# Kernel tuning notes

Measured on AMD Instinct MI355X. Metric: run time of the kernel, lower is better.

Reference implementation:

```python
import jax, jax.numpy as jnp
import numpy as np

N_NODES = 100000


def gcn_conv(x, W, b, row, col, n_nodes):
    # Symmetric GCN normalization without self-loops (add_self_loops=False):
    # deg[i] = number of incoming edges at target i (edge_weight = 1)
    deg = jax.ops.segment_sum(jnp.ones(row.shape[0], dtype=x.dtype), col,
                              num_segments=n_nodes)
    dinv = jnp.where(deg > 0, jax.lax.rsqrt(jnp.maximum(deg, 1.0)), 0.0)
    norm = dinv[row] * dinv[col]  # [E]
    h = x @ W                      # [N, out] linear transform first (PyG order)
    msg = h[row] * norm[:, None]   # gather + scale, [E, out]
    out = jax.ops.segment_sum(msg, col, num_segments=n_nodes)  # scatter-add
    return out + b


def setup_inputs() -> dict:
    key = jax.random.key(0)
    k1, k2, k3, k4, k5, k6 = jax.random.split(key, 6)
    n, in_c, hid, out_c, e = N_NODES, 128, 32, 16, 3200000
    x = jax.random.normal(k1, (n, in_c), dtype=jnp.float32)
    edge_index = jax.random.randint(k2, (2, e), 0, n, dtype=jnp.int64)
    # Glorot-style init for GCN weights, zeros bias (PyG default)
    W1 = jax.random.normal(k3, (in_c, hid), dtype=jnp.float32) / np.sqrt(in_c)
    b1 = jnp.zeros((hid,), dtype=jnp.float32)
    W2 = jax.random.normal(k4, (hid, out_c), dtype=jnp.float32) / np.sqrt(hid)
    b2 = jnp.zeros((out_c,), dtype=jnp.float32)
    return {"x": x, "edge_index": edge_index, "W1": W1, "b1": b1,
            "W2": W2, "b2": b2}


def reference(x, edge_index, W1, b1, W2, b2):
    row, col = edge_index[0], edge_index[1]
    h = gcn_conv(x, W1, b1, row, col, N_NODES)
    h = jax.nn.relu(h)
    out = gcn_conv(h, W2, b2, row, col, N_NODES)
    return (out, 0)
```

## Files before the change

### kernel.cpp

```cpp
#include <hip/hip_runtime.h>


#define WAVE 64
#define BN2 512
#define NBMAX 256
#define CHUNK 8192

typedef _Float16 f16;

__global__ void bucket_count_kernel(const int* __restrict__ col, int* __restrict__ gcnt,
                                    int E, int nb) {
    __shared__ int h[NBMAX];
    for (int i = threadIdx.x; i < nb; i += blockDim.x) h[i] = 0;
    __syncthreads();
    for (int e = blockIdx.x * blockDim.x + threadIdx.x; e < E; e += gridDim.x * blockDim.x)
        atomicAdd(&h[col[e] >> 9], 1);
    __syncthreads();
    for (int i = threadIdx.x; i < nb; i += blockDim.x)
        if (h[i]) atomicAdd(&gcnt[i], h[i]);
}

__global__ void bucket_scan_kernel(const int* __restrict__ cnt, int* __restrict__ bptr,
                                   int* __restrict__ gcur, int nb, int* __restrict__ gpcur,
                                   f16* __restrict__ hlo, f16* __restrict__ hhi,
                                   f16* __restrict__ h2t, int nzr) {
    int lane = threadIdx.x;
    if (lane == 0) gpcur[0] = 0;
    if (lane < 16)      hlo[(size_t)nzr * 16 + lane]        = (f16)0.f;
    else if (lane < 32) hhi[(size_t)nzr * 16 + (lane - 16)] = (f16)0.f;
    else if (lane < 48) h2t[(size_t)nzr * 16 + (lane - 32)] = (f16)0.f;
    int carry = 0;
    for (int base = 0; base < nb; base += WAVE) {
        int i = base + lane;
        int orig = (i < nb) ? cnt[i] : 0;
        int v = orig;
#pragma unroll
        for (int off = 1; off < WAVE; off <<= 1) {
            int t = __shfl_up(v, off, WAVE);
            if (lane >= off) v += t;
        }
        if (i < nb) { bptr[i] = carry + v - orig; gcur[i] = carry + v - orig; }
        carry += __shfl(v, WAVE - 1, WAVE);
    }
    if (lane == 0) bptr[nb] = carry;
}

__global__ void __launch_bounds__(512)
partition_kernel(const int* __restrict__ row, const int* __restrict__ col,
                 int* __restrict__ gcursor, unsigned* __restrict__ packed,
                 int E, int nb) {
    __shared__ int hist[NBMAX], excl[NBMAX], cursor[NBMAX], baseoff[NBMAX];
    __shared__ unsigned stage[CHUNK];
    int chunk0 = blockIdx.x * CHUNK;
    int cn = E - chunk0; if (cn > CHUNK) cn = CHUNK;
    for (int i = threadIdx.x; i < nb; i += blockDim.x) hist[i] = 0;
    __syncthreads();
    for (int i = threadIdx.x; i < cn; i += blockDim.x)
        atomicAdd(&hist[col[chunk0 + i] >> 9], 1);
    __syncthreads();
    if (threadIdx.x < WAVE) {
        int lane = threadIdx.x, carry = 0;
        for (int base = 0; base < nb; base += WAVE) {
            int i = base + lane;
            int orig = (i < nb) ? hist[i] : 0;
            int v = orig;
#pragma unroll
            for (int off = 1; off < WAVE; off <<= 1) {
                int t = __shfl_up(v, off, WAVE);
                if (lane >= off) v += t;
            }
            if (i < nb) { excl[i] = carry + v - orig; cursor[i] = carry + v - orig; }
            carry += __shfl(v, WAVE - 1, WAVE);
        }
    }
    __syncthreads();
    for (int b = threadIdx.x; b < nb; b += blockDim.x) {
        int c = hist[b];
        baseoff[b] = c ? atomicAdd(&gcursor[b], c) : 0;
    }
    __syncthreads();
    for (int i = threadIdx.x; i < cn; i += blockDim.x) {
        int c = col[chunk0 + i], r = row[chunk0 + i];
        int b = c >> 9;
        int pos = atomicAdd(&cursor[b], 1);
        stage[pos] = ((unsigned)r << 9) | (unsigned)(c & (BN2 - 1));
    }
    __syncthreads();
    int wave = threadIdx.x >> 6, lane = threadIdx.x & 63, nw = blockDim.x >> 6;
    for (int b = wave; b < nb; b += nw) {
        int c = hist[b]; if (!c) continue;
        int s = excl[b], d = baseoff[b];
        for (int k = lane; k < c; k += WAVE) packed[d + k] = stage[s + k];
    }
}

__global__ void __launch_bounds__(512)
sort_kernel(const int* __restrict__ bptr, const unsigned* __restrict__ packed,
            int* __restrict__ srcs, int2* __restrict__ pse,
            float* __restrict__ dinv, int* __restrict__ gpcur,
            int n, int nb, int E) {
    __shared__ int hist[BN2], pex[BN2], cur[BN2];
    __shared__ int pbase_s;
    int b = blockIdx.x;
    int start = bptr[b], end = bptr[b + 1];
    for (int i = threadIdx.x; i < BN2; i += blockDim.x) { hist[i] = 0; cur[i] = 0; }
    __syncthreads();
    for (int k = start + threadIdx.x; k < end; k += blockDim.x)
        atomicAdd(&hist[packed[k] & (BN2 - 1)], 1);
    __syncthreads();
    if (threadIdx.x < WAVE) {
        int lane = threadIdx.x, carry = 0;
#pragma unroll
        for (int base = 0; base < BN2; base += WAVE) {
            int i = base + lane;
            int pd = (hist[i] + 15) & ~15;
            int v = pd;
#pragma unroll
            for (int off = 1; off < WAVE; off <<= 1) {
                int t = __shfl_up(v, off, WAVE);
                if (lane >= off) v += t;
            }
            pex[i] = carry + v - pd;
            carry += __shfl(v, WAVE - 1, WAVE);
        }
        if (lane == 0) pbase_s = atomicAdd(gpcur, carry);
    }
    __syncthreads();
    int pbase = pbase_s;
    for (int i = threadIdx.x; i < BN2; i += blockDim.x) {
        int node = b * BN2 + i;
        if (node < n) {
            int d = hist[i], pd = (d + 15) & ~15;
            int ps = pbase + pex[i];
            pse[node]  = d ? make_int2(ps, ps + pd) : make_int2(0, 0);
            dinv[node] = d ? rsqrtf((float)d) : 0.f;
            for (int k = d; k < pd; ++k) srcs[ps + k] = n;
        }
    }
    __syncthreads();
    for (int k = start + threadIdx.x; k < end; k += blockDim.x) {
        unsigned p = packed[k];
        int lc = p & (BN2 - 1);
        int pos = atomicAdd(&cur[lc], 1);
        srcs[pbase + pex[lc] + pos] = (int)(p >> 9);
    }
}

template <int INC, int OUTC, int JT, bool SPLIT>
__global__ void __launch_bounds__(256, 4)
dense_kernel(const float* __restrict__ x, const float* __restrict__ W,
             const float* __restrict__ dinv, f16* __restrict__ hlo,
             f16* __restrict__ hhi, int n) {
    const int LSTR = INC + 4;
    const int SP   = 256 / JT;
    const int NT   = SP * 2;
    __shared__ float Wt[OUTC * LSTR];
    for (int i = threadIdx.x; i < INC * OUTC; i += 256) {
        int k = i / OUTC, j = i % OUTC;
        Wt[j * LSTR + k] = W[i];
    }
    __syncthreads();
    const int jg = threadIdx.x % JT;
    const int sp = threadIdx.x / JT;
    int base = blockIdx.x * NT;
    int n0 = base + sp;
    int n1 = base + sp + SP;
    int n0c = n0 < n ? n0 : n - 1;
    int n1c = n1 < n ? n1 : n - 1;
    const float4* xr0 = (const float4*)(x + (size_t)n0c * INC);
    const float4* xr1 = (const float4*)(x + (size_t)n1c * INC);
    float a[2][4] = {{0.f, 0.f, 0.f, 0.f}, {0.f, 0.f, 0.f, 0.f}};
#pragma unroll 4
    for (int k4 = 0; k4 < INC / 4; ++k4) {
        float4 v0 = xr0[k4];
        float4 v1 = xr1[k4];
#pragma unroll
        for (int u = 0; u < 4; ++u) {
            float4 w = *(const float4*)(Wt + (jg + u * JT) * LSTR + 4 * k4);
            a[0][u] = fmaf(v0.x, w.x, fmaf(v0.y, w.y, fmaf(v0.z, w.z, fmaf(v0.w, w.w, a[0][u]))));
            a[1][u] = fmaf(v1.x, w.x, fmaf(v1.y, w.y, fmaf(v1.z, w.z, fmaf(v1.w, w.w, a[1][u]))));
        }
    }
#pragma unroll
    for (int pair = 0; pair < 2; ++pair) {
        int nn = pair ? n1 : n0;
        if (nn < n) {
            float d = dinv[nn];
#pragma unroll
            for (int u = 0; u < 4; ++u) {
                int c = jg + u * JT;
                f16* t;
                if (SPLIT) t = (c < 16) ? (hlo + (size_t)nn * 16 + c)
                               : (hhi + (size_t)nn * 16 + (c - 16));
                else       t = hlo + (size_t)nn * OUTC + c;
                *t = (f16)(a[pair][u] * d);
            }
        }
    }
}

#define GLD(s) (*(const f16*)(hb + (((unsigned)(s) << 5) + j2)))

template <bool RELU>
__global__ void __launch_bounds__(256)
csr_agg16x2_kernel(const int2* __restrict__ pse, const int* __restrict__ srcs,
                   const float* __restrict__ dinv, const f16* __restrict__ tlo,
                   const f16* __restrict__ thi, const float* __restrict__ bias,
                   float* __restrict__ out, int ostride, int hg, int n, int tailidx) {
    int bid = blockIdx.x;
    int pass = (bid >= hg) ? 1 : 0;
    const f16* hs = pass ? thi : tlo;
    int ocol = pass << 4;
    int bip = bid - pass * hg;
    int lane = threadIdx.x & 63;
    int wid  = threadIdx.x >> 6;
    int j  = lane & 15;
    int eo = lane >> 4;
    if (tailidx >= 0 && bid == 0 && threadIdx.x == 0) out[tailidx] = 0.f;
    int n0 = (bip * 4 + wid) * 2;
    if (n0 >= n) return;
    int n1 = n0 + 1;
    bool v1 = n1 < n;
    int4 se = *(const int4*)(pse + n0);
    int nb0 = (se.y - se.x) >> 4;
    int nb1 = v1 ? ((se.w - se.z) >> 4) : 0;
    float dv0 = dinv[n0];
    float dv1 = v1 ? dinv[n1] : 0.f;
    float bj = bias[ocol + j];
    size_t ob0 = (size_t)n0 * ostride + ocol + j;
    size_t ob1 = (size_t)n1 * ostride + ocol + j;
    int MAXB = nb0 > nb1 ? nb0 : nb1;
    if (MAXB == 0) {
        float v = bj;
        if (RELU) v = v > 0.f ? v : 0.f;
        if (eo == 0) out[ob0] = v;
        else if (eo == 1 && v1) out[ob1] = v;
        return;
    }
    const unsigned j2 = (unsigned)(j << 1);
    const char* hb = (const char*)hs;
    const int4* P0 = (const int4*)(srcs + se.x) + eo;
    const int4* P1 = (const int4*)(srcs + (v1 ? se.z : se.x)) + eo;
    int nc0 = nb0 > 1 ? nb0 : 1;
    int nc1 = nb1 > 1 ? nb1 : 1;
    int4 sA0 = P0[0];
    int4 sA1 = P1[0];
    f16 h0 = GLD(sA0.x), h1 = GLD(sA0.y), h2 = GLD(sA0.z), h3 = GLD(sA0.w);
    f16 h4 = GLD(sA1.x), h5 = GLD(sA1.y), h6 = GLD(sA1.z), h7 = GLD(sA1.w);
    int4 sB0 = P0[(nc0 > 1 ? 1 : 0) * 4];
    int4 sB1 = P1[(nc1 > 1 ? 1 : 0) * 4];
    float acc0 = 0.f, acc1 = 0.f, acc2 = 0.f, acc3 = 0.f;
    for (int b = 0; b < MAXB - 1; ++b) {
        f16 g0 = GLD(sB0.x), g1 = GLD(sB0.y), g2 = GLD(sB0.z), g3 = GLD(sB0.w);
        f16 g4 = GLD(sB1.x), g5 = GLD(sB1.y), g6 = GLD(sB1.z), g7 = GLD(sB1.w);
        int x0 = (b + 2) < nc0 ? (b + 2) : nc0 - 1;
        int x1 = (b + 2) < nc1 ? (b + 2) : nc1 - 1;
        int4 t0 = P0[x0 * 4];
        int4 t1 = P1[x1 * 4];
        float m0 = b < nb0 ? 1.f : 0.f;
        float m1 = b < nb1 ? 1.f : 0.f;
        acc0 = fmaf(m0, (float)h0, acc0);
        acc1 = fmaf(m0, (float)h1, acc1);
        acc0 = fmaf(m0, (float)h2, acc0);
        acc1 = fmaf(m0, (float)h3, acc1);
        acc2 = fmaf(m1, (float)h4, acc2);
        acc3 = fmaf(m1, (float)h5, acc3);
        acc2 = fmaf(m1, (float)h6, acc2);
        acc3 = fmaf(m1, (float)h7, acc3);
        h0 = g0; h1 = g1; h2 = g2; h3 = g3;
        h4 = g4; h5 = g5; h6 = g6; h7 = g7;
        sB0 = t0; sB1 = t1;
    }
    {
        float m0 = (MAXB - 1) < nb0 ? 1.f : 0.f;
        float m1 = (MAXB - 1) < nb1 ? 1.f : 0.f;
        acc0 = fmaf(m0, (float)h0, acc0);
        acc1 = fmaf(m0, (float)h1, acc1);
        acc0 = fmaf(m0, (float)h2, acc0);
        acc1 = fmaf(m0, (float)h3, acc1);
        acc2 = fmaf(m1, (float)h4, acc2);
        acc3 = fmaf(m1, (float)h5, acc3);
        acc2 = fmaf(m1, (float)h6, acc2);
        acc3 = fmaf(m1, (float)h7, acc3);
    }
    float accA = acc0 + acc1;
    float accB = acc2 + acc3;
    accA += __shfl_xor(accA, 16, WAVE);
    accA += __shfl_xor(accA, 32, WAVE);
    accB += __shfl_xor(accB, 16, WAVE);
    accB += __shfl_xor(accB, 32, WAVE);
    if (eo == 0) {
        float v = accA * dv0 + bj;
        if (RELU) v = v > 0.f ? v : 0.f;
        out[ob0] = v;
    } else if (eo == 1 && v1) {
        float v = accB * dv1 + bj;
        if (RELU) v = v > 0.f ? v : 0.f;
        out[ob1] = v;
    }
}

extern "C" void kernel_launch(void* const* d_in, const int* in_sizes, int n_in,
                              void* d_out, int out_size, void* d_ws, size_t ws_size,
                              hipStream_t stream) {
    const float* x  = (const float*)d_in[0];
    const int*   ei = (const int*)d_in[1];
    const float* W1 = (const float*)d_in[2];
    const float* b1 = (const float*)d_in[3];
    const float* W2 = (const float*)d_in[4];
    const float* b2 = (const float*)d_in[5];

    const int IN_C = 128, HID = 32, OC = 16;
    const int N = in_sizes[0] / IN_C;
    const int E = in_sizes[1] / 2;
    const int* row = ei;
    const int* col = ei + E;
    const int NB = (N + BN2 - 1) / BN2;

    char* base = (char*)d_ws;
    size_t off = 0;
    auto carve = [&](size_t bytes) -> char* {
        char* p = base + off;
        off = (off + bytes + 255) & ~(size_t)255;
        return p;
    };
    int*      gcnt  = (int*)     carve((size_t)NB * 4);
    int*      bptr  = (int*)     carve((size_t)(NB + 1) * 4);
    int*      gcur  = (int*)     carve((size_t)NB * 4);
    int*      gpcur = (int*)     carve(8);
    float*    dinv  = (float*)   carve((size_t)N * 4);
    int2*     pse   = (int2*)    carve((size_t)(N + 2) * 8);
    unsigned* packed= (unsigned*)carve((size_t)E * 4);
    int*      srcsP = (int*)     carve(((size_t)E + (size_t)N * 32 + 256) * 4);
    f16*      hlo   = (f16*)     carve((size_t)(N + 1) * 16 * 2);
    f16*      hhi   = (f16*)     carve((size_t)(N + 1) * 16 * 2);
    f16*      h2t   = (f16*)     carve((size_t)(N + 1) * 16 * 2);
    float*    bufB  = (float*)   carve((size_t)N * HID * 4);
    (void)ws_size; (void)n_in;

    float* outp = (float*)d_out;

    hipMemsetAsync(gcnt, 0, (size_t)NB * 4, stream);
    bucket_count_kernel<<<512, 256, 0, stream>>>(col, gcnt, E, NB);
    bucket_scan_kernel<<<1, 64, 0, stream>>>(gcnt, bptr, gcur, NB, gpcur, hlo, hhi, h2t, N);
    partition_kernel<<<(E + CHUNK - 1) / CHUNK, 512, 0, stream>>>(row, col, gcur, packed, E, NB);
    sort_kernel<<<NB, 512, 0, stream>>>(bptr, packed, srcsP, pse, dinv, gpcur, N, NB, E);

    int npb = 8;
    int g2  = (N + npb - 1) / npb;

    {
        const int NT = (256 / 8) * 2;
        dense_kernel<128, 32, 8, true><<<(N + NT - 1) / NT, 256, 0, stream>>>(x, W1, dinv, hlo, hhi, N);
        csr_agg16x2_kernel<true><<<2 * g2, 256, 0, stream>>>(
            pse, srcsP, dinv, hlo, hhi, b1, bufB, HID, g2, N, -1);
    }
    {
        const int NT = (256 / 4) * 2;
        dense_kernel<32, 16, 4, false><<<(N + NT - 1) / NT, 256, 0, stream>>>(bufB, W2, dinv, h2t, nullptr, N);
        int tailidx = (out_size > N * OC) ? (N * OC) : -1;
        csr_agg16x2_kernel<false><<<g2, 256, 0, stream>>>(
            pse, srcsP, dinv, h2t, h2t, b2, outp, OC, g2, N, tailidx);
    }
}
```

Measured before the change: 192.0 us.

## Merge split layer-1 feature halves into one 32-column fp16 aggregation pass

After: 182.3 us. 5.0% less time.

```diff
diff --git a/kernel.cpp b/kernel.cpp
--- a/kernel.cpp
+++ b/kernel.cpp
@@ -22,12 +22,10 @@
 
 __global__ void bucket_scan_kernel(const int* __restrict__ cnt, int* __restrict__ bptr,
                                    int* __restrict__ gcur, int nb, int* __restrict__ gpcur,
-                                   f16* __restrict__ hlo, f16* __restrict__ hhi,
-                                   f16* __restrict__ h2t, int nzr) {
+                                   f16* __restrict__ hA, f16* __restrict__ h2t, int nzr) {
     int lane = threadIdx.x;
     if (lane == 0) gpcur[0] = 0;
-    if (lane < 16)      hlo[(size_t)nzr * 16 + lane]        = (f16)0.f;
-    else if (lane < 32) hhi[(size_t)nzr * 16 + (lane - 16)] = (f16)0.f;
+    if (lane < 32)      hA[(size_t)nzr * 32 + lane]         = (f16)0.f;
     else if (lane < 48) h2t[(size_t)nzr * 16 + (lane - 32)] = (f16)0.f;
     int carry = 0;
     for (int base = 0; base < nb; base += WAVE) {
@@ -146,11 +144,10 @@
     }
 }
 
-template <int INC, int OUTC, int JT, bool SPLIT>
+template <int INC, int OUTC, int JT>
 __global__ void __launch_bounds__(256, 4)
 dense_kernel(const float* __restrict__ x, const float* __restrict__ W,
-             const float* __restrict__ dinv, f16* __restrict__ hlo,
-             f16* __restrict__ hhi, int n) {
+             const float* __restrict__ dinv, f16* __restrict__ h, int n) {
     const int LSTR = INC + 4;
     const int SP   = 256 / JT;
     const int NT   = SP * 2;
@@ -186,38 +183,121 @@
         int nn = pair ? n1 : n0;
         if (nn < n) {
             float d = dinv[nn];
-#pragma unroll
-            for (int u = 0; u < 4; ++u) {
-                int c = jg + u * JT;
-                f16* t;
-                if (SPLIT) t = (c < 16) ? (hlo + (size_t)nn * 16 + c)
-                               : (hhi + (size_t)nn * 16 + (c - 16));
-                else       t = hlo + (size_t)nn * OUTC + c;
-                *t = (f16)(a[pair][u] * d);
-            }
-        }
-    }
-}
-
-#define GLD(s) (*(const f16*)(hb + (((unsigned)(s) << 5) + j2)))
+            f16* hr = h + (size_t)nn * OUTC;
+#pragma unroll
+            for (int u = 0; u < 4; ++u) hr[jg + u * JT] = (f16)(a[pair][u] * d);
+        }
+    }
+}
+
+#define GLD32(s) (*(const f16*)(hb + (((unsigned)(s) << 6) + j2)))
+
+template <bool RELU>
+__global__ void __launch_bounds__(256)
+csr_agg32x2_kernel(const int2* __restrict__ pse, const int* __restrict__ srcs,
+                   const float* __restrict__ dinv, const f16* __restrict__ hs,
+                   const float* __restrict__ bias, float* __restrict__ out,
+                   int ostride, int n) {
+    int lane = threadIdx.x & 63;
+    int wid  = threadIdx.x >> 6;
+    int j  = lane & 31;
+    int eo = lane >> 5;
+    int n0 = ((int)blockIdx.x * 4 + wid) * 2;
+    if (n0 >= n) return;
+    int n1 = n0 + 1;
+    bool v1 = n1 < n;
+    int4 se = *(const int4*)(pse + n0);
+    int nb0 = (se.y - se.x) >> 3;
+    int nb1 = v1 ? ((se.w - se.z) >> 3) : 0;
+    float dv0 = dinv[n0];
+    float dv1 = v1 ? dinv[n1] : 0.f;
+    float bj = bias[j];
+    size_t ob0 = (size_t)n0 * ostride + j;
+    size_t ob1 = (size_t)n1 * ostride + j;
+    int MAXB = nb0 > nb1 ? nb0 : nb1;
+    if (MAXB == 0) {
+        float v = bj;
+        if (RELU) v = v > 0.f ? v : 0.f;
+        if (eo == 0) out[ob0] = v;
+        else if (v1) out[ob1] = v;
+        return;
+    }
+    const unsigned j2 = (unsigned)(j << 1);
+    const char* hb = (const char*)hs;
+    const int4* P0 = (const int4*)(srcs + se.x) + eo;
+    const int4* P1 = (const int4*)(srcs + (v1 ? se.z : se.x)) + eo;
+    int nc0 = nb0 > 1 ? nb0 : 1;
+    int nc1 = nb1 > 1 ? nb1 : 1;
+    int4 sA0 = P0[0];
+    int4 sA1 = P1[0];
+    f16 h0 = GLD32(sA0.x), h1 = GLD32(sA0.y), h2 = GLD32(sA0.z), h3 = GLD32(sA0.w);
+    f16 h4 = GLD32(sA1.x), h5 = GLD32(sA1.y), h6 = GLD32(sA1.z), h7 = GLD32(sA1.w);
+    int4 sB0 = P0[(nc0 > 1 ? 1 : 0) * 2];
+    int4 sB1 = P1[(nc1 > 1 ? 1 : 0) * 2];
+    float acc0 = 0.f, acc1 = 0.f, acc2 = 0.f, acc3 = 0.f;
+    for (int b = 0; b < MAXB - 1; ++b) {
+        f16 g0 = GLD32(sB0.x), g1 = GLD32(sB0.y), g2 = GLD32(sB0.z), g3 = GLD32(sB0.w);
+        f16 g4 = GLD32(sB1.x), g5 = GLD32(sB1.y), g6 = GLD32(sB1.z), g7 = GLD32(sB1.w);
+        int x0 = (b + 2) < nc0 ? (b + 2) : nc0 - 1;
+        int x1 = (b + 2) < nc1 ? (b + 2) : nc1 - 1;
+        int4 t0 = P0[x0 * 2];
+        int4 t1 = P1[x1 * 2];
+        float m0 = b < nb0 ? 1.f : 0.f;
+        float m1 = b < nb1 ? 1.f : 0.f;
+        acc0 = fmaf(m0, (float)h0, acc0);
+        acc1 = fmaf(m0, (float)h1, acc1);
+        acc0 = fmaf(m0, (float)h2, acc0);
+        acc1 = fmaf(m0, (float)h3, acc1);
+        acc2 = fmaf(m1, (float)h4, acc2);
+        acc3 = fmaf(m1, (float)h5, acc3);
+        acc2 = fmaf(m1, (float)h6, acc2);
+        acc3 = fmaf(m1, (float)h7, acc3);
+        h0 = g0; h1 = g1; h2 = g2; h3 = g3;
+        h4 = g4; h5 = g5; h6 = g6; h7 = g7;
+        sB0 = t0; sB1 = t1;
+    }
+    {
+        float m0 = (MAXB - 1) < nb0 ? 1.f : 0.f;
+        float m1 = (MAXB - 1) < nb1 ? 1.f : 0.f;
+        acc0 = fmaf(m0, (float)h0, acc0);
+        acc1 = fmaf(m0, (float)h1, acc1);
+        acc0 = fmaf(m0, (float)h2, acc0);
+        acc1 = fmaf(m0, (float)h3, acc1);
+        acc2 = fmaf(m1, (float)h4, acc2);
+        acc3 = fmaf(m1, (float)h5, acc3);
+        acc2 = fmaf(m1, (float)h6, acc2);
+        acc3 = fmaf(m1, (float)h7, acc3);
+    }
+    float accA = acc0 + acc1;
+    float accB = acc2 + acc3;
+    accA += __shfl_xor(accA, 32, WAVE);
+    accB += __shfl_xor(accB, 32, WAVE);
+    if (eo == 0) {
+        float v = accA * dv0 + bj;
+        if (RELU) v = v > 0.f ? v : 0.f;
+        out[ob0] = v;
+    } else if (v1) {
+        float v = accB * dv1 + bj;
+        if (RELU) v = v > 0.f ? v : 0.f;
+        out[ob1] = v;
+    }
+}
+
+#define GLD16(s) (*(const f16*)(hb + (((unsigned)(s) << 5) + j2)))
 
 template <bool RELU>
 __global__ void __launch_bounds__(256)
 csr_agg16x2_kernel(const int2* __restrict__ pse, const int* __restrict__ srcs,
-                   const float* __restrict__ dinv, const f16* __restrict__ tlo,
-                   const f16* __restrict__ thi, const float* __restrict__ bias,
-                   float* __restrict__ out, int ostride, int hg, int n, int tailidx) {
+                   const float* __restrict__ dinv, const f16* __restrict__ hs,
+                   const float* __restrict__ bias, float* __restrict__ out,
+                   int ostride, int n, int tailidx) {
     int bid = blockIdx.x;
-    int pass = (bid >= hg) ? 1 : 0;
-    const f16* hs = pass ? thi : tlo;
-    int ocol = pass << 4;
-    int bip = bid - pass * hg;
     int lane = threadIdx.x & 63;
     int wid  = threadIdx.x >> 6;
     int j  = lane & 15;
     int eo = lane >> 4;
     if (tailidx >= 0 && bid == 0 && threadIdx.x == 0) out[tailidx] = 0.f;
-    int n0 = (bip * 4 + wid) * 2;
+    int n0 = (bid * 4 + wid) * 2;
     if (n0 >= n) return;
     int n1 = n0 + 1;
     bool v1 = n1 < n;
@@ -226,9 +306,9 @@
     int nb1 = v1 ? ((se.w - se.z) >> 4) : 0;
     float dv0 = dinv[n0];
     float dv1 = v1 ? dinv[n1] : 0.f;
-    float bj = bias[ocol + j];
-    size_t ob0 = (size_t)n0 * ostride + ocol + j;
-    size_t ob1 = (size_t)n1 * ostride + ocol + j;
+    float bj = bias[j];
+    size_t ob0 = (size_t)n0 * ostride + j;
+    size_t ob1 = (size_t)n1 * ostride + j;
     int MAXB = nb0 > nb1 ? nb0 : nb1;
     if (MAXB == 0) {
         float v = bj;
@@ -245,14 +325,14 @@
     int nc1 = nb1 > 1 ? nb1 : 1;
     int4 sA0 = P0[0];
     int4 sA1 = P1[0];
-    f16 h0 = GLD(sA0.x), h1 = GLD(sA0.y), h2 = GLD(sA0.z), h3 = GLD(sA0.w);
-    f16 h4 = GLD(sA1.x), h5 = GLD(sA1.y), h6 = GLD(sA1.z), h7 = GLD(sA1.w);
+    f16 h0 = GLD16(sA0.x), h1 = GLD16(sA0.y), h2 = GLD16(sA0.z), h3 = GLD16(sA0.w);
+    f16 h4 = GLD16(sA1.x), h5 = GLD16(sA1.y), h6 = GLD16(sA1.z), h7 = GLD16(sA1.w);
     int4 sB0 = P0[(nc0 > 1 ? 1 : 0) * 4];
     int4 sB1 = P1[(nc1 > 1 ? 1 : 0) * 4];
     float acc0 = 0.f, acc1 = 0.f, acc2 = 0.f, acc3 = 0.f;
     for (int b = 0; b < MAXB - 1; ++b) {
-        f16 g0 = GLD(sB0.x), g1 = GLD(sB0.y), g2 = GLD(sB0.z), g3 = GLD(sB0.w);
-        f16 g4 = GLD(sB1.x), g5 = GLD(sB1.y), g6 = GLD(sB1.z), g7 = GLD(sB1.w);
+        f16 g0 = GLD16(sB0.x), g1 = GLD16(sB0.y), g2 = GLD16(sB0.z), g3 = GLD16(sB0.w);
+        f16 g4 = GLD16(sB1.x), g5 = GLD16(sB1.y), g6 = GLD16(sB1.z), g7 = GLD16(sB1.w);
         int x0 = (b + 2) < nc0 ? (b + 2) : nc0 - 1;
         int x1 = (b + 2) < nc1 ? (b + 2) : nc1 - 1;
         int4 t0 = P0[x0 * 4];
@@ -332,8 +412,7 @@
     int2*     pse   = (int2*)    carve((size_t)(N + 2) * 8);
     unsigned* packed= (unsigned*)carve((size_t)E * 4);
     int*      srcsP = (int*)     carve(((size_t)E + (size_t)N * 32 + 256) * 4);
-    f16*      hlo   = (f16*)     carve((size_t)(N + 1) * 16 * 2);
-    f16*      hhi   = (f16*)     carve((size_t)(N + 1) * 16 * 2);
+    f16*      hA    = (f16*)     carve((size_t)(N + 1) * 32 * 2);
     f16*      h2t   = (f16*)     carve((size_t)(N + 1) * 16 * 2);
     float*    bufB  = (float*)   carve((size_t)N * HID * 4);
     (void)ws_size; (void)n_in;
@@ -342,7 +421,7 @@
 
     hipMemsetAsync(gcnt, 0, (size_t)NB * 4, stream);
     bucket_count_kernel<<<512, 256, 0, stream>>>(col, gcnt, E, NB);
-    bucket_scan_kernel<<<1, 64, 0, stream>>>(gcnt, bptr, gcur, NB, gpcur, hlo, hhi, h2t, N);
+    bucket_scan_kernel<<<1, 64, 0, stream>>>(gcnt, bptr, gcur, NB, gpcur, hA, h2t, N);
     partition_kernel<<<(E + CHUNK - 1) / CHUNK, 512, 0, stream>>>(row, col, gcur, packed, E, NB);
     sort_kernel<<<NB, 512, 0, stream>>>(bptr, packed, srcsP, pse, dinv, gpcur, N, NB, E);
 
@@ -351,15 +430,15 @@
 
     {
         const int NT = (256 / 8) * 2;
-        dense_kernel<128, 32, 8, true><<<(N + NT - 1) / NT, 256, 0, stream>>>(x, W1, dinv, hlo, hhi, N);
-        csr_agg16x2_kernel<true><<<2 * g2, 256, 0, stream>>>(
-            pse, srcsP, dinv, hlo, hhi, b1, bufB, HID, g2, N, -1);
+        dense_kernel<128, 32, 8><<<(N + NT - 1) / NT, 256, 0, stream>>>(x, W1, dinv, hA, N);
+        csr_agg32x2_kernel<true><<<g2, 256, 0, stream>>>(
+            pse, srcsP, dinv, hA, b1, bufB, HID, N);
     }
     {
         const int NT = (256 / 4) * 2;
-        dense_kernel<32, 16, 4, false><<<(N + NT - 1) / NT, 256, 0, stream>>>(bufB, W2, dinv, h2t, nullptr, N);
+        dense_kernel<32, 16, 4><<<(N + NT - 1) / NT, 256, 0, stream>>>(bufB, W2, dinv, h2t, N);
         int tailidx = (out_size > N * OC) ? (N * OC) : -1;
         csr_agg16x2_kernel<false><<<g2, 256, 0, stream>>>(
-            pse, srcsP, dinv, h2t, h2t, b2, outp, OC, g2, N, tailidx);
-    }
-}
+            pse, srcsP, dinv, h2t, b2, outp, OC, N, tailidx);
+    }
+}
```
